# Optimization experiments

Measured on AMD Instinct MI355X. Metric: run time of the kernel, lower is better.

The kernel has to match this reference:

```python
import jax, jax.numpy as jnp
import numpy as np

BITS = 4
MAXQ = 15           # 2**BITS - 1
PACK = 32 // BITS   # 8 nibbles per int32
GROUP = 128         # quantization group size along in_features


def _unpack_rows(packed, rows):
    """Unpack int32-packed 4-bit values along axis 0. packed: [Kp, N] -> [rows, N]."""
    shifts = jnp.arange(0, 32, BITS, dtype=jnp.int32)            # [PACK]
    u = (packed[:, None, :] >> shifts[None, :, None]) & MAXQ    # [Kp, PACK, N]
    return u.reshape(-1, packed.shape[1])[:rows]


def _unpack_cols(packed, cols):
    """Unpack int32-packed 4-bit values along axis 1. packed: [G, Np] -> [G, cols]."""
    shifts = jnp.arange(0, 32, BITS, dtype=jnp.int32)            # [PACK]
    u = (packed[:, :, None] >> shifts[None, None, :]) & MAXQ    # [G, Np, PACK]
    return u.reshape(packed.shape[0], -1)[:, :cols]


def setup_inputs() -> dict:
    key = jax.random.key(0)
    k1, k2, k3, k4, k5 = jax.random.split(key, 5)
    K, N = 4096, 11008
    x = jax.random.normal(k1, (4, 2048, K), dtype=jnp.float32)
    qweight = jax.random.randint(k2, (K // PACK, N), 0, 2**31 - 1, dtype=jnp.int32)
    scales = jax.random.uniform(k3, (K // GROUP, N), dtype=jnp.float32)
    qzeros = jax.random.randint(k4, (K // GROUP, (N + PACK - 1) // PACK), 0, 2**31 - 1, dtype=jnp.int32)
    bias = jax.random.normal(k5, (N,), dtype=jnp.float32)
    return {"x": x, "qweight": qweight, "scales": scales, "qzeros": qzeros, "bias": bias}


def reference(x, qweight, scales, qzeros, bias):
    K = x.shape[-1]
    N = scales.shape[1]
    qw = _unpack_rows(qweight, K)            # [K, N] int in [0, 15]
    qz = _unpack_cols(qzeros, N) + 1         # [G, N] int in [1, 16] (+1 per get_unpacked_params)
    s = jnp.repeat(scales, GROUP, axis=0)    # [K, N]  groupwise -> per-row
    z = jnp.repeat(qz, GROUP, axis=0)        # [K, N]
    W = (qw - z).astype(x.dtype) * s         # dequantized weight [K, N]
    out = jnp.matmul(x, W) + bias
    return out.astype(x.dtype)
```

## Files before the change

kernel.cpp:

```cpp
#include <hip/hip_runtime.h>
#include <hip/hip_bf16.h>
#include <stdint.h>

typedef __attribute__((ext_vector_type(4))) float f32x4;
typedef __attribute__((ext_vector_type(8))) short bf16x8;
typedef __attribute__((ext_vector_type(8))) unsigned short ushort8;
typedef __attribute__((ext_vector_type(4))) unsigned short ushort4v;

__device__ __forceinline__ unsigned short f2bf(float f) {
    union { float f; unsigned int u; } v; v.f = f;
    unsigned int u = v.u;
    u += 0x7FFFu + ((u >> 16) & 1u);
    return (unsigned short)(u >> 16);
}

__device__ __forceinline__ int swz(int row, int k) {
    return (row * 64 + k) ^ ((row & 7) << 3);
}

__device__ __forceinline__ void gld16(const void* g, void* l) {
    __builtin_amdgcn_global_load_lds(
        (const __attribute__((address_space(1))) unsigned int*)g,
        (__attribute__((address_space(3))) unsigned int*)l,
        16, 0, 0);
}

__global__ __launch_bounds__(256)
void cvt_x(const float* __restrict__ X, unsigned short* __restrict__ Xb, long long n8) {
    long long i0 = (long long)blockIdx.x * 256 + threadIdx.x;
    long long stride = (long long)gridDim.x * 256;
    for (long long i = i0; i < n8; i += stride) {
        const float4* p = reinterpret_cast<const float4*>(X + i * 8);
        float4 a = p[0], b = p[1];
        ushort8 o;
        o[0] = f2bf(a.x); o[1] = f2bf(a.y); o[2] = f2bf(a.z); o[3] = f2bf(a.w);
        o[4] = f2bf(b.x); o[5] = f2bf(b.y); o[6] = f2bf(b.z); o[7] = f2bf(b.w);
        *reinterpret_cast<ushort8*>(Xb + i * 8) = o;
    }
}

__global__ __launch_bounds__(256)
void deq_w(const int* __restrict__ QW, const float* __restrict__ SC,
           const int* __restrict__ QZ, unsigned short* __restrict__ WT,
           int N, int K) {
    const int ntiles = N >> 6;
    const int nb = blockIdx.x % ntiles;
    const int kb = blockIdx.x / ntiles;
    const int n0 = nb * 64, kp0 = kb * 64;
    const int t = threadIdx.x;
    #pragma unroll
    for (int w = 0; w < 16; ++w) {
        const int p = t + 256 * w;
        const int kpo = p & 63, ni = p >> 6;
        const int n = n0 + ni, kp = kp0 + kpo;
        const int g = kp >> 4;
        const float s = SC[(size_t)g * N + n];
        const int zq = ((QZ[(size_t)g * (N >> 3) + (n >> 3)] >> ((n & 7) * 4)) & 15) + 1;
        const float zb = -(float)zq * s;
        const unsigned int q = (unsigned int)QW[(size_t)kp * N + n];
        ushort8 o;
        #pragma unroll
        for (int j = 0; j < 8; ++j)
            o[j] = f2bf(fmaf((float)((q >> (4 * j)) & 15u), s, zb));
        *reinterpret_cast<ushort8*>(&WT[(size_t)n * K + kp * 8]) = o;
    }
}

__global__ __launch_bounds__(512, 2)
void qgemm_256(const unsigned short* __restrict__ Xb, const unsigned short* __restrict__ WT,
               const float* __restrict__ BIAS, float* __restrict__ OUT,
               int M, int N, int K) {
    __shared__ __align__(16) unsigned short S[65536];

    int id = blockIdx.x;
    const int nwg = gridDim.x;
    if ((nwg & 7) == 0) id = (id & 7) * (nwg >> 3) + (id >> 3);

    const int ntn = N >> 8;
    const int bm = (id / ntn) << 8;
    const int bn = (id % ntn) << 8;
    const int tid = threadIdx.x;
    const int lane = tid & 63;
    const int wid = tid >> 6;
    const int wm = (wid >> 2) * 64;
    const int wn = (wid & 3) * 32;
    const int lr = lane & 15;
    const int lk = (lane >> 4) * 8;

    f32x4 acc[8][4] = {};
    const int nk = K >> 6;

    auto stage_half = [&](int cur, int t, int kind, int half) {
        const unsigned short* gb = (kind ? WT + (size_t)(bn + half * 128) * K
                                         : Xb + (size_t)(bm + half * 128) * K) + (size_t)t * 64;
        unsigned short* lb = S + (kind ? 32768 : 0) + cur * 16384 + half * 8192;
        #pragma unroll
        for (int r = 0; r < 2; ++r) {
            const int s = r * 512 + tid;
            const int row = s >> 3, c8 = s & 7;
            gld16(gb + (size_t)row * K + ((c8 ^ (row & 7)) << 3), lb + s * 8);
        }
    };

    bf16x8 aL[4][2], aH[4][2], bL[2][2], bH[2][2];

    auto loadA = [&](bf16x8 (&dst)[4][2], const unsigned short* Sa, int rbase) {
        #pragma unroll
        for (int i = 0; i < 4; ++i)
            #pragma unroll
            for (int kk = 0; kk < 2; ++kk)
                dst[i][kk] = *reinterpret_cast<const bf16x8*>(&Sa[swz(rbase + i * 16 + lr, kk * 32 + lk)]);
    };
    auto loadB = [&](bf16x8 (&dst)[2][2], const unsigned short* Sb, int rbase) {
        #pragma unroll
        for (int j = 0; j < 2; ++j)
            #pragma unroll
            for (int kk = 0; kk < 2; ++kk)
                dst[j][kk] = *reinterpret_cast<const bf16x8*>(&Sb[swz(rbase + j * 16 + lr, kk * 32 + lk)]);
    };
    auto quad = [&](bf16x8 (&A)[4][2], bf16x8 (&B)[2][2], int mi0, int nj0) {
        __builtin_amdgcn_s_setprio(1);
        #pragma unroll
        for (int kk = 0; kk < 2; ++kk)
            #pragma unroll
            for (int i = 0; i < 4; ++i)
                #pragma unroll
                for (int j = 0; j < 2; ++j)
                    acc[mi0 + i][nj0 + j] = __builtin_amdgcn_mfma_f32_16x16x32_bf16(
                        A[i][kk], B[j][kk], acc[mi0 + i][nj0 + j], 0, 0, 0);
        __builtin_amdgcn_s_setprio(0);
    };

    stage_half(0, 0, 0, 0); stage_half(0, 0, 0, 1);
    stage_half(0, 0, 1, 0); stage_half(0, 0, 1, 1);
    stage_half(1, 1, 0, 0); stage_half(1, 1, 0, 1); stage_half(1, 1, 1, 0);
    asm volatile("s_waitcnt vmcnt(6)" ::: "memory");
    __builtin_amdgcn_s_barrier();

    for (int t = 0; t < nk; ++t) {
        const int cur = t & 1;
        const unsigned short* Sa = S + cur * 16384;
        const unsigned short* Sb = S + 32768 + cur * 16384;

        loadA(aL, Sa, wm);
        loadB(bL, Sb, wn);
        if (t + 1 < nk) stage_half(cur ^ 1, t + 1, 1, 1);
        __builtin_amdgcn_s_barrier();
        asm volatile("s_waitcnt lgkmcnt(0)" ::: "memory");
        quad(aL, bL, 0, 0);
        __builtin_amdgcn_s_barrier();

        loadA(aH, Sa, 128 + wm);
        if (t + 2 < nk) stage_half(cur, t + 2, 0, 0);
        __builtin_amdgcn_s_barrier();
        asm volatile("s_waitcnt lgkmcnt(0)" ::: "memory");
        quad(aH, bL, 4, 0);
        __builtin_amdgcn_s_barrier();

        loadB(bH, Sb, 128 + wn);
        if (t + 2 < nk) stage_half(cur, t + 2, 0, 1);
        __builtin_amdgcn_s_barrier();
        asm volatile("s_waitcnt lgkmcnt(0)" ::: "memory");
        quad(aL, bH, 0, 2);
        __builtin_amdgcn_s_barrier();

        if (t + 2 < nk) {
            stage_half(cur, t + 2, 1, 0);
            asm volatile("s_waitcnt vmcnt(6)" ::: "memory");
        } else {
            asm volatile("s_waitcnt vmcnt(0)" ::: "memory");
        }
        __builtin_amdgcn_s_barrier();
        quad(aH, bH, 4, 2);
        __builtin_amdgcn_s_barrier();
    }

    #pragma unroll
    for (int mi = 0; mi < 8; ++mi) {
        const int row = bm + wm + (mi & 3) * 16 + ((mi >> 2) ? 128 : 0) + (lane >> 4) * 4;
        #pragma unroll
        for (int nj = 0; nj < 4; ++nj) {
            const int col = bn + wn + (nj & 1) * 16 + ((nj >> 1) ? 128 : 0) + lr;
            const float b = BIAS[col];
            #pragma unroll
            for (int r = 0; r < 4; ++r)
                OUT[(size_t)(row + r) * N + col] = acc[mi][nj][r] + b;
        }
    }
}

__global__ __launch_bounds__(256, 2)
void qgemm_ws(const unsigned short* __restrict__ Xb, const unsigned short* __restrict__ WT,
              const float* __restrict__ BIAS, float* __restrict__ OUT,
              int M, int N, int K) {
    __shared__ __align__(16) unsigned short As[2][128 * 64];
    __shared__ __align__(16) unsigned short Bs[2][128 * 64];

    const int ntn = N >> 7;
    const int bm = (blockIdx.x / ntn) * 128;
    const int bn = (blockIdx.x % ntn) * 128;
    const int tid = threadIdx.x;
    const int lane = tid & 63;
    const int wave = tid >> 6;
    const int wm = (wave >> 1) * 64, wn = (wave & 1) * 64;
    const int lr = lane & 15, lk = (lane >> 4) * 8;

    f32x4 acc[4][4] = {};
    const int nk = K >> 6;

    auto stage = [&](int buf, int t) {
        const int k0 = t * 64;
        #pragma unroll
        for (int p = 0; p < 4; ++p) {
            const int slot = p * 256 + tid;
            const int row = slot >> 3, c = slot & 7;
            const int gk = k0 + ((c ^ (row & 7)) << 3);
            gld16(Xb + (size_t)(bm + row) * K + gk, &As[buf][slot * 8]);
            gld16(WT + (size_t)(bn + row) * K + gk, &Bs[buf][slot * 8]);
        }
    };

    auto compute = [&](int buf) {
        #pragma unroll
        for (int kk = 0; kk < 2; ++kk) {
            bf16x8 af[4], bfr[4];
            #pragma unroll
            for (int i = 0; i < 4; ++i) {
                af[i]  = *reinterpret_cast<const bf16x8*>(&As[buf][swz(wm + i * 16 + lr, kk * 32 + lk)]);
                bfr[i] = *reinterpret_cast<const bf16x8*>(&Bs[buf][swz(wn + i * 16 + lr, kk * 32 + lk)]);
            }
            #pragma unroll
            for (int i = 0; i < 4; ++i)
                #pragma unroll
                for (int j = 0; j < 4; ++j)
                    acc[i][j] = __builtin_amdgcn_mfma_f32_16x16x32_bf16(af[i], bfr[j], acc[i][j], 0, 0, 0);
        }
    };

    stage(0, 0);
    __syncthreads();
    int cur = 0;
    for (int t = 0; t < nk; ++t) {
        if (t + 1 < nk) stage(cur ^ 1, t + 1);
        compute(cur);
        __syncthreads();
        cur ^= 1;
    }

    #pragma unroll
    for (int i = 0; i < 4; ++i) {
        #pragma unroll
        for (int j = 0; j < 4; ++j) {
            const int col = bn + wn + j * 16 + lr;
            const float b = BIAS[col];
            #pragma unroll
            for (int r = 0; r < 4; ++r) {
                const int row = bm + wm + i * 16 + (lane >> 4) * 4 + r;
                OUT[(size_t)row * N + col] = acc[i][j][r] + b;
            }
        }
    }
}

__global__ __launch_bounds__(256, 2)
void qgemm_fb(const float* __restrict__ X, const int* __restrict__ QW,
              const float* __restrict__ SC, const int* __restrict__ QZ,
              const float* __restrict__ BIAS, float* __restrict__ OUT,
              int M, int N, int K) {
    __shared__ __align__(16) unsigned short As[2][128 * 64];
    __shared__ __align__(16) unsigned short Bs[2][128 * 64];

    const int ntn = N / 128;
    const int bm = (blockIdx.x / ntn) * 128;
    const int bn = (blockIdx.x % ntn) * 128;
    const int tid  = threadIdx.x;
    const int lane = tid & 63;
    const int wave = tid >> 6;
    const int wm = (wave >> 1) * 64, wn = (wave & 1) * 64;
    const int lr = lane & 15, lk = (lane >> 4) * 8;
    const int a_c4 = tid & 15, a_r0 = tid >> 4;
    const int b_n  = tid & 127, b_k0 = tid >> 7;

    f32x4 acc[4][4] = {};
    float4 va[8];
    unsigned int wb[4];
    float sc_s = 0.f, sc_zb = 0.f;
    const int nk = K / 64;

    auto gload = [&](int t) {
        const int k0 = t * 64;
        #pragma unroll
        for (int p = 0; p < 8; ++p)
            va[p] = *reinterpret_cast<const float4*>(X + (size_t)(bm + a_r0 + p * 16) * K + k0 + a_c4 * 4);
        const int g  = k0 >> 7;
        const int gn = bn + b_n;
        sc_s = SC[(size_t)g * N + gn];
        const int zq = ((QZ[(size_t)g * (N >> 3) + (gn >> 3)] >> ((gn & 7) * 4)) & 15) + 1;
        sc_zb = -(float)zq * sc_s;
        #pragma unroll
        for (int p = 0; p < 4; ++p)
            wb[p] = (unsigned int)QW[(size_t)(t * 8 + b_k0 + p * 2) * N + gn];
    };

    auto lwrite = [&](int buf) {
        #pragma unroll
        for (int p = 0; p < 8; ++p) {
            const int row = a_r0 + p * 16;
            ushort4v b;
            b.x = f2bf(va[p].x); b.y = f2bf(va[p].y);
            b.z = f2bf(va[p].z); b.w = f2bf(va[p].w);
            *reinterpret_cast<ushort4v*>(&As[buf][swz(row, a_c4 * 4)]) = b;
        }
        #pragma unroll
        for (int p = 0; p < 4; ++p) {
            const int ko = b_k0 + p * 2;
            ushort8 o;
            #pragma unroll
            for (int j = 0; j < 8; ++j)
                o[j] = f2bf(fmaf((float)((wb[p] >> (4 * j)) & 15u), sc_s, sc_zb));
            *reinterpret_cast<ushort8*>(&Bs[buf][swz(b_n, ko * 8)]) = o;
        }
    };

    auto compute = [&](int buf) {
        #pragma unroll
        for (int kk = 0; kk < 2; ++kk) {
            bf16x8 af[4], bfr[4];
            #pragma unroll
            for (int i = 0; i < 4; ++i) {
                af[i]  = *reinterpret_cast<const bf16x8*>(&As[buf][swz(wm + i * 16 + lr, kk * 32 + lk)]);
                bfr[i] = *reinterpret_cast<const bf16x8*>(&Bs[buf][swz(wn + i * 16 + lr, kk * 32 + lk)]);
            }
            #pragma unroll
            for (int i = 0; i < 4; ++i)
                #pragma unroll
                for (int j = 0; j < 4; ++j)
                    acc[i][j] = __builtin_amdgcn_mfma_f32_16x16x32_bf16(af[i], bfr[j], acc[i][j], 0, 0, 0);
        }
    };

    gload(0); lwrite(0);
    __syncthreads();
    for (int t = 0; t < nk; ++t) {
        if (t + 1 < nk) gload(t + 1);
        compute(t & 1);
        if (t + 1 < nk) lwrite((t + 1) & 1);
        __syncthreads();
    }

    #pragma unroll
    for (int i = 0; i < 4; ++i) {
        #pragma unroll
        for (int j = 0; j < 4; ++j) {
            const int col = bn + wn + j * 16 + lr;
            const float b = BIAS[col];
            #pragma unroll
            for (int r = 0; r < 4; ++r) {
                const int row = bm + wm + i * 16 + (lane >> 4) * 4 + r;
                OUT[(size_t)row * N + col] = acc[i][j][r] + b;
            }
        }
    }
}

extern "C" void kernel_launch(void* const* d_in, const int* in_sizes, int n_in,
                              void* d_out, int out_size, void* d_ws, size_t ws_size,
                              hipStream_t stream) {
    const float* X    = (const float*)d_in[0];
    const int*   QW   = (const int*)d_in[1];
    const float* SC   = (const float*)d_in[2];
    const int*   QZ   = (const int*)d_in[3];
    const float* BIAS = (const float*)d_in[4];
    float* OUT = (float*)d_out;

    const int N = in_sizes[4];
    const long long qwsz = in_sizes[1];
    const int K = (int)(qwsz * 8 / N);
    const int M = in_sizes[0] / K;

    const size_t xb_bytes = (size_t)M * K * 2;
    const size_t wt_bytes = (size_t)N * K * 2;

    if (ws_size >= xb_bytes + wt_bytes) {
        unsigned short* Xb = (unsigned short*)d_ws;
        unsigned short* WT = Xb + (size_t)M * K;

        cvt_x<<<2048, 256, 0, stream>>>(X, Xb, (long long)M * K / 8);
        deq_w<<<(N >> 6) * (K / 512), 256, 0, stream>>>(QW, SC, QZ, WT, N, K);

        if ((M % 256) == 0 && (N % 256) == 0 && (K % 64) == 0 && (K / 64) >= 4) {
            qgemm_256<<<(M / 256) * (N / 256), 512, 0, stream>>>(Xb, WT, BIAS, OUT, M, N, K);
        } else {
            qgemm_ws<<<(M / 128) * (N / 128), 256, 0, stream>>>(Xb, WT, BIAS, OUT, M, N, K);
        }
    } else {
        qgemm_fb<<<(M / 128) * (N / 128), 256, 0, stream>>>(X, QW, SC, QZ, BIAS, OUT, M, N, K);
    }
}
```

Measured before the change: 769.7 us.

## Switch 256x256 GEMM to 32x32x16 MFMA with K-split phases and constexpr shapes

Replaces the 16x16x32 bf16 MFMA tiling with 32x32x16 MFMA fragments, so each wave keeps 4x2 f32x16 accumulators. The 64-wide K step is now processed in two K halves, each split into low and high M phases, and the global-to-LDS prefetch schedule is reordered to issue both halves of the next tile together. K and N become template constants specialised for 4096x11008, which removes runtime index arithmetic. The larger MFMA is meant to raise math throughput per LDS read, at the cost of a different register footprint and a dispatch that only covers this exact shape.

```diff
diff --git a/kernel.cpp b/kernel.cpp
--- a/kernel.cpp
+++ b/kernel.cpp
@@ -3,6 +3,7 @@
 #include <stdint.h>
 
 typedef __attribute__((ext_vector_type(4))) float f32x4;
+typedef __attribute__((ext_vector_type(16))) float f32x16;
 typedef __attribute__((ext_vector_type(8))) short bf16x8;
 typedef __attribute__((ext_vector_type(8))) unsigned short ushort8;
 typedef __attribute__((ext_vector_type(4))) unsigned short ushort4v;
@@ -66,17 +67,17 @@
     }
 }
 
+template<int KC, int NC>
 __global__ __launch_bounds__(512, 2)
 void qgemm_256(const unsigned short* __restrict__ Xb, const unsigned short* __restrict__ WT,
-               const float* __restrict__ BIAS, float* __restrict__ OUT,
-               int M, int N, int K) {
+               const float* __restrict__ BIAS, float* __restrict__ OUT, int M) {
     __shared__ __align__(16) unsigned short S[65536];
 
     int id = blockIdx.x;
     const int nwg = gridDim.x;
     if ((nwg & 7) == 0) id = (id & 7) * (nwg >> 3) + (id >> 3);
 
-    const int ntn = N >> 8;
+    constexpr int ntn = NC >> 8;
     const int bm = (id / ntn) << 8;
     const int bn = (id % ntn) << 8;
     const int tid = threadIdx.x;
@@ -84,107 +85,146 @@
     const int wid = tid >> 6;
     const int wm = (wid >> 2) * 64;
     const int wn = (wid & 3) * 32;
-    const int lr = lane & 15;
-    const int lk = (lane >> 4) * 8;
-
-    f32x4 acc[8][4] = {};
-    const int nk = K >> 6;
-
-    auto stage_half = [&](int cur, int t, int kind, int half) {
-        const unsigned short* gb = (kind ? WT + (size_t)(bn + half * 128) * K
-                                         : Xb + (size_t)(bm + half * 128) * K) + (size_t)t * 64;
-        unsigned short* lb = S + (kind ? 32768 : 0) + cur * 16384 + half * 8192;
+    const int l31 = lane & 31;
+    const int kb8 = (lane >> 5) * 8;
+
+    f32x16 acc[4][2] = {};
+    constexpr int nk = KC >> 6;
+
+    auto stage_half = [&](int buf, int t, int kind, int half) {
+        const unsigned short* gb = (kind ? WT + (size_t)(bn + half * 128) * KC
+                                         : Xb + (size_t)(bm + half * 128) * KC) + (size_t)t * 64;
+        unsigned short* lb = S + (kind ? 32768 : 0) + buf * 16384 + half * 8192;
         #pragma unroll
         for (int r = 0; r < 2; ++r) {
             const int s = r * 512 + tid;
             const int row = s >> 3, c8 = s & 7;
-            gld16(gb + (size_t)row * K + ((c8 ^ (row & 7)) << 3), lb + s * 8);
-        }
-    };
-
-    bf16x8 aL[4][2], aH[4][2], bL[2][2], bH[2][2];
-
-    auto loadA = [&](bf16x8 (&dst)[4][2], const unsigned short* Sa, int rbase) {
-        #pragma unroll
-        for (int i = 0; i < 4; ++i)
-            #pragma unroll
-            for (int kk = 0; kk < 2; ++kk)
-                dst[i][kk] = *reinterpret_cast<const bf16x8*>(&Sa[swz(rbase + i * 16 + lr, kk * 32 + lk)]);
-    };
-    auto loadB = [&](bf16x8 (&dst)[2][2], const unsigned short* Sb, int rbase) {
-        #pragma unroll
-        for (int j = 0; j < 2; ++j)
-            #pragma unroll
-            for (int kk = 0; kk < 2; ++kk)
-                dst[j][kk] = *reinterpret_cast<const bf16x8*>(&Sb[swz(rbase + j * 16 + lr, kk * 32 + lk)]);
-    };
-    auto quad = [&](bf16x8 (&A)[4][2], bf16x8 (&B)[2][2], int mi0, int nj0) {
-        __builtin_amdgcn_s_setprio(1);
-        #pragma unroll
-        for (int kk = 0; kk < 2; ++kk)
-            #pragma unroll
-            for (int i = 0; i < 4; ++i)
-                #pragma unroll
-                for (int j = 0; j < 2; ++j)
-                    acc[mi0 + i][nj0 + j] = __builtin_amdgcn_mfma_f32_16x16x32_bf16(
-                        A[i][kk], B[j][kk], acc[mi0 + i][nj0 + j], 0, 0, 0);
-        __builtin_amdgcn_s_setprio(0);
+            gld16(gb + (size_t)row * KC + ((c8 ^ (row & 7)) << 3), lb + s * 8);
+        }
+    };
+
+    auto rdA = [&](const unsigned short* Sa, int mf, int kk) -> bf16x8 {
+        const int row = ((mf >> 1) * 128) + wm + ((mf & 1) * 32) + l31;
+        return *reinterpret_cast<const bf16x8*>(&Sa[swz(row, kk * 16 + kb8)]);
+    };
+    auto rdB = [&](const unsigned short* Sb, int nf, int kk) -> bf16x8 {
+        const int row = nf * 128 + wn + l31;
+        return *reinterpret_cast<const bf16x8*>(&Sb[swz(row, kk * 16 + kb8)]);
     };
 
     stage_half(0, 0, 0, 0); stage_half(0, 0, 0, 1);
     stage_half(0, 0, 1, 0); stage_half(0, 0, 1, 1);
-    stage_half(1, 1, 0, 0); stage_half(1, 1, 0, 1); stage_half(1, 1, 1, 0);
-    asm volatile("s_waitcnt vmcnt(6)" ::: "memory");
+    if (nk > 1) { stage_half(1, 1, 0, 0); stage_half(1, 1, 1, 0); }
+    asm volatile("s_waitcnt vmcnt(4)" ::: "memory");
     __builtin_amdgcn_s_barrier();
 
     for (int t = 0; t < nk; ++t) {
-        const int cur = t & 1;
-        const unsigned short* Sa = S + cur * 16384;
-        const unsigned short* Sb = S + 32768 + cur * 16384;
-
-        loadA(aL, Sa, wm);
-        loadB(bL, Sb, wn);
-        if (t + 1 < nk) stage_half(cur ^ 1, t + 1, 1, 1);
+        const int c = t & 1;
+        const unsigned short* Sa = S + c * 16384;
+        const unsigned short* Sb = S + 32768 + c * 16384;
+
+        bf16x8 aLo[2][2], aHi[2][2], bb[2][2];
+
+        #pragma unroll
+        for (int mf = 0; mf < 2; ++mf)
+            #pragma unroll
+            for (int kk = 0; kk < 2; ++kk) aLo[mf][kk] = rdA(Sa, mf, kk);
+        #pragma unroll
+        for (int nf = 0; nf < 2; ++nf)
+            #pragma unroll
+            for (int kk = 0; kk < 2; ++kk) bb[nf][kk] = rdB(Sb, nf, kk);
+        if (t + 1 < nk) { stage_half(c ^ 1, t + 1, 0, 1); stage_half(c ^ 1, t + 1, 1, 1); }
         __builtin_amdgcn_s_barrier();
         asm volatile("s_waitcnt lgkmcnt(0)" ::: "memory");
-        quad(aL, bL, 0, 0);
-        __builtin_amdgcn_s_barrier();
-
-        loadA(aH, Sa, 128 + wm);
-        if (t + 2 < nk) stage_half(cur, t + 2, 0, 0);
+        __builtin_amdgcn_s_setprio(1);
+        #pragma unroll
+        for (int kk = 0; kk < 2; ++kk)
+            #pragma unroll
+            for (int mf = 0; mf < 2; ++mf)
+                #pragma unroll
+                for (int nf = 0; nf < 2; ++nf)
+                    acc[mf][nf] = __builtin_amdgcn_mfma_f32_32x32x16_bf16(
+                        aLo[mf][kk], bb[nf][kk], acc[mf][nf], 0, 0, 0);
+        __builtin_amdgcn_s_setprio(0);
+        __builtin_amdgcn_s_barrier();
+
+        #pragma unroll
+        for (int mf = 0; mf < 2; ++mf)
+            #pragma unroll
+            for (int kk = 0; kk < 2; ++kk) aHi[mf][kk] = rdA(Sa, 2 + mf, kk);
         __builtin_amdgcn_s_barrier();
         asm volatile("s_waitcnt lgkmcnt(0)" ::: "memory");
-        quad(aH, bL, 4, 0);
-        __builtin_amdgcn_s_barrier();
-
-        loadB(bH, Sb, 128 + wn);
-        if (t + 2 < nk) stage_half(cur, t + 2, 0, 1);
+        __builtin_amdgcn_s_setprio(1);
+        #pragma unroll
+        for (int kk = 0; kk < 2; ++kk)
+            #pragma unroll
+            for (int mf = 0; mf < 2; ++mf)
+                #pragma unroll
+                for (int nf = 0; nf < 2; ++nf)
+                    acc[2 + mf][nf] = __builtin_amdgcn_mfma_f32_32x32x16_bf16(
+                        aHi[mf][kk], bb[nf][kk], acc[2 + mf][nf], 0, 0, 0);
+        __builtin_amdgcn_s_setprio(0);
+        __builtin_amdgcn_s_barrier();
+
+        #pragma unroll
+        for (int mf = 0; mf < 2; ++mf)
+            #pragma unroll
+            for (int kk = 0; kk < 2; ++kk) aLo[mf][kk] = rdA(Sa, mf, 2 + kk);
+        #pragma unroll
+        for (int nf = 0; nf < 2; ++nf)
+            #pragma unroll
+            for (int kk = 0; kk < 2; ++kk) bb[nf][kk] = rdB(Sb, nf, 2 + kk);
         __builtin_amdgcn_s_barrier();
         asm volatile("s_waitcnt lgkmcnt(0)" ::: "memory");
-        quad(aL, bH, 0, 2);
-        __builtin_amdgcn_s_barrier();
-
+        __builtin_amdgcn_s_setprio(1);
+        #pragma unroll
+        for (int kk = 0; kk < 2; ++kk)
+            #pragma unroll
+            for (int mf = 0; mf < 2; ++mf)
+                #pragma unroll
+                for (int nf = 0; nf < 2; ++nf)
+                    acc[mf][nf] = __builtin_amdgcn_mfma_f32_32x32x16_bf16(
+                        aLo[mf][kk], bb[nf][kk], acc[mf][nf], 0, 0, 0);
+        __builtin_amdgcn_s_setprio(0);
+        __builtin_amdgcn_s_barrier();
+
+        #pragma unroll
+        for (int mf = 0; mf < 2; ++mf)
+            #pragma unroll
+            for (int kk = 0; kk < 2; ++kk) aHi[mf][kk] = rdA(Sa, 2 + mf, 2 + kk);
         if (t + 2 < nk) {
-            stage_half(cur, t + 2, 1, 0);
-            asm volatile("s_waitcnt vmcnt(6)" ::: "memory");
+            stage_half(c, t + 2, 0, 0); stage_half(c, t + 2, 1, 0);
+            asm volatile("s_waitcnt vmcnt(4)" ::: "memory");
         } else {
             asm volatile("s_waitcnt vmcnt(0)" ::: "memory");
         }
         __builtin_amdgcn_s_barrier();
-        quad(aH, bH, 4, 2);
+        asm volatile("s_waitcnt lgkmcnt(0)" ::: "memory");
+        __builtin_amdgcn_s_setprio(1);
+        #pragma unroll
+        for (int kk = 0; kk < 2; ++kk)
+            #pragma unroll
+            for (int mf = 0; mf < 2; ++mf)
+                #pragma unroll
+                for (int nf = 0; nf < 2; ++nf)
+                    acc[2 + mf][nf] = __builtin_amdgcn_mfma_f32_32x32x16_bf16(
+                        aHi[mf][kk], bb[nf][kk], acc[2 + mf][nf], 0, 0, 0);
+        __builtin_amdgcn_s_setprio(0);
         __builtin_amdgcn_s_barrier();
     }
 
     #pragma unroll
-    for (int mi = 0; mi < 8; ++mi) {
-        const int row = bm + wm + (mi & 3) * 16 + ((mi >> 2) ? 128 : 0) + (lane >> 4) * 4;
-        #pragma unroll
-        for (int nj = 0; nj < 4; ++nj) {
-            const int col = bn + wn + (nj & 1) * 16 + ((nj >> 1) ? 128 : 0) + lr;
-            const float b = BIAS[col];
-            #pragma unroll
-            for (int r = 0; r < 4; ++r)
-                OUT[(size_t)(row + r) * N + col] = acc[mi][nj][r] + b;
+    for (int mf = 0; mf < 4; ++mf) {
+        const int rb = bm + (mf >> 1) * 128 + wm + (mf & 1) * 32 + (lane >> 5) * 4;
+        #pragma unroll
+        for (int nf = 0; nf < 2; ++nf) {
+            const int col = bn + nf * 128 + wn + l31;
+            const float bv = BIAS[col];
+            #pragma unroll
+            for (int q = 0; q < 4; ++q)
+                #pragma unroll
+                for (int r = 0; r < 4; ++r)
+                    OUT[(size_t)(rb + q * 8 + r) * NC + col] = acc[mf][nf][q * 4 + r] + bv;
         }
     }
 }
@@ -388,8 +428,8 @@
         cvt_x<<<2048, 256, 0, stream>>>(X, Xb, (long long)M * K / 8);
         deq_w<<<(N >> 6) * (K / 512), 256, 0, stream>>>(QW, SC, QZ, WT, N, K);
 
-        if ((M % 256) == 0 && (N % 256) == 0 && (K % 64) == 0 && (K / 64) >= 4) {
-            qgemm_256<<<(M / 256) * (N / 256), 512, 0, stream>>>(Xb, WT, BIAS, OUT, M, N, K);
+        if (K == 4096 && N == 11008 && (M % 256) == 0) {
+            qgemm_256<4096, 11008><<<(M / 256) * (11008 / 256), 512, 0, stream>>>(Xb, WT, BIAS, OUT, M);
         } else {
             qgemm_ws<<<(M / 128) * (N / 128), 256, 0, stream>>>(Xb, WT, BIAS, OUT, M, N, K);
         }
```

Result: slower. 900.1 us (+16.9%).
